# Kernel optimization log

Hardware: AMD Instinct MI355X
Metric: run time of the kernel (lower is better)

The kernel has to match this reference:

```python
import jax, jax.numpy as jnp
import numpy as np
import math

NUM_HEADS = 8
C_RATIO = 0.5

def _dwconv(x, w, b, pad):
    # x: [B,C,H,W], w: [C,1,kh,kw] depthwise
    y = jax.lax.conv_general_dilated(x, w, (1, 1), [(pad, pad), (pad, pad)],
                                     dimension_numbers=('NCHW', 'OIHW', 'NCHW'),
                                     feature_group_count=x.shape[1])
    return y + b[None, :, None, None]

def setup_inputs():
    key = jax.random.key(0)
    ks = jax.random.split(key, 16)
    B, H, W, C = 2, 128, 128, 384
    cr = int(C * C_RATIO)  # 192
    cg = C // 3            # 128
    s = 0.02
    return {
        'x': jax.random.normal(ks[0], (B, H * W, C), jnp.float32),
        'red_w1': jax.random.normal(ks[1], (cg, 1, 1, 1), jnp.float32) * s,
        'red_b1': jnp.zeros((cg,), jnp.float32),
        'red_w3': jax.random.normal(ks[2], (cg, 1, 3, 3), jnp.float32) * s,
        'red_b3': jnp.zeros((cg,), jnp.float32),
        'red_w5': jax.random.normal(ks[3], (cg, 1, 5, 5), jnp.float32) * s,
        'red_b5': jnp.zeros((cg,), jnp.float32),
        'fus_w': jax.random.normal(ks[4], (cr, C, 4, 4), jnp.float32) * s,
        'fus_b': jnp.zeros((cr,), jnp.float32),
        'q_w': jax.random.normal(ks[5], (C, cr), jnp.float32) * s,
        'k_w': jax.random.normal(ks[6], (cr, cr), jnp.float32) * s,
        'v_w': jax.random.normal(ks[7], (cr, C), jnp.float32) * s,
        'cpe_w': jax.random.normal(ks[8], (C, 1, 3, 3), jnp.float32) * s,
        'cpe_b': jnp.zeros((C,), jnp.float32),
        'proj_w': jax.random.normal(ks[9], (C, C), jnp.float32) * s,
        'proj_b': jnp.zeros((C,), jnp.float32),
        'H': 128,
        'W': 128,
    }

def reference(x, red_w1, red_b1, red_w3, red_b3, red_w5, red_b5,
              fus_w, fus_b, q_w, k_w, v_w, cpe_w, cpe_b, proj_w, proj_b, H, W):
    B, N, C = x.shape
    cr = q_w.shape[1]
    hd = C // NUM_HEADS
    dk = cr // NUM_HEADS
    scale = (hd * C_RATIO) ** -0.5
    _time = max(int(math.log(H // 16, 4)), int(math.log(W // 16, 4)))
    _scale = 4 ** _time  # == 4 for our shapes

    _x = x.transpose(0, 2, 1).reshape(B, C, H, W)
    x1, x2, x3 = jnp.split(_x, 3, axis=1)
    y1 = _dwconv(x1, red_w1, red_b1, 0)                       # applied once
    y2 = _dwconv(_dwconv(x2, red_w3, red_b3, 1), red_w3, red_b3, 1)  # twice
    y3 = x3
    for _ in range(3):                                        # thrice
        y3 = _dwconv(y3, red_w5, red_b5, 2)
    fused = jnp.concatenate([y1, y2, y3], axis=1)             # [B,C,H,W]

    f = jax.lax.conv_general_dilated(fused, fus_w, (4, 4), [(0, 0), (0, 0)],
                                     dimension_numbers=('NCHW', 'OIHW', 'NCHW'))
    f = jax.nn.gelu(f + fus_b[None, :, None, None], approximate=False)
    _xr = f.reshape(B, cr, -1).transpose(0, 2, 1)             # [B, L, cr], L = (H/4)*(W/4)

    q = (x @ q_w).reshape(B, N, NUM_HEADS, dk).transpose(0, 2, 1, 3)    # [B,h,N,dk]
    k = (_xr @ k_w).reshape(B, -1, NUM_HEADS, dk).transpose(0, 2, 1, 3) # [B,h,L,dk]
    v = (_xr @ v_w).reshape(B, -1, NUM_HEADS, hd).transpose(0, 2, 1, 3) # [B,h,L,hd]

    attn = jax.nn.softmax(jnp.einsum('bhnd,bhld->bhnl', q, k) * scale, axis=-1)

    Hs, Ws = H // _scale, W // _scale
    v_sp = v.transpose(0, 2, 1, 3).reshape(B, -1, C).transpose(0, 2, 1).reshape(B, C, Hs, Ws)
    v = v + _dwconv(v_sp, cpe_w, cpe_b, 1).reshape(B, C, -1).reshape(
        B, NUM_HEADS, hd, -1).transpose(0, 1, 3, 2)

    out = jnp.einsum('bhnl,bhld->bhnd', attn, v).transpose(0, 2, 1, 3).reshape(B, N, C)
    return out @ proj_w + proj_b
```

## Files before the change

kernel.cpp:

```cpp
#include <hip/hip_runtime.h>
#include <math.h>

typedef short short8 __attribute__((ext_vector_type(8)));
typedef float f32x4 __attribute__((ext_vector_type(4)));

#define B_    2
#define HH    128
#define WW    128
#define NPIX  16384
#define C_    384
#define CR    192
#define CG    128
#define NH    8
#define DK    24
#define HD    48
#define LL    1024
#define KFUS  6144
#define SCALE_L2E 0.29448889f

__device__ __forceinline__ float bf2f(short h) {
    union { unsigned u; float f; } v; v.u = ((unsigned)(unsigned short)h) << 16; return v.f;
}
__device__ __forceinline__ short f2bf(float f) {
    union { float f; unsigned u; } v; v.f = f;
    unsigned r = v.u + 0x7fffu + ((v.u >> 16) & 1u);
    return (short)(unsigned short)(r >> 16);
}
__device__ __forceinline__ short f2bf_fast(float f) {
    union { float f; unsigned u; } v; v.f = f;
    return (short)(unsigned short)((v.u + 0x8000u) >> 16);
}
__device__ __forceinline__ float exp2b(float x) {
#if __has_builtin(__builtin_amdgcn_exp2f)
    return __builtin_amdgcn_exp2f(x);
#else
    return exp2f(x);
#endif
}
__device__ __forceinline__ unsigned cvt_pk_bf16(float lo, float hi) {
    unsigned r;
    asm("v_cvt_pk_bf16_f32 %0, %1, %2" : "=v"(r) : "v"(lo), "v"(hi));
    return r;
}

template<int PATCH, int KS, int STRIDE>
__global__ __launch_bounds__(256) void dwconv_k(
    const float* __restrict__ in, int in_off,
    float* __restrict__ outf, short* __restrict__ outp, int out_coff,
    const float* __restrict__ w, const float* __restrict__ bias)
{
    constexpr int pad = KS / 2;
    constexpr int NV = 4 + KS - 1;
    int idx = blockIdx.x * 256 + threadIdx.x;
    int c    = idx & (CG - 1);
    int pix4 = (idx >> 7) & 4095;
    int b    = idx >> 19;
    int y = pix4 >> 5, x0 = (pix4 & 31) << 2;
    float wl[KS * KS];
    #pragma unroll
    for (int i = 0; i < KS * KS; i++) wl[i] = w[c * KS * KS + i];
    float bv = bias[c];
    float acc[4] = {bv, bv, bv, bv};
    #pragma unroll
    for (int ky = 0; ky < KS; ky++) {
        int yy = y + ky - pad;
        if ((unsigned)yy >= HH) continue;
        const float* rowp = &in[(size_t)(b * NPIX + yy * WW) * STRIDE + in_off + c];
        float v[NV];
        #pragma unroll
        for (int j = 0; j < NV; j++) {
            int xx = x0 + j - pad;
            v[j] = ((unsigned)xx < WW) ? rowp[(size_t)xx * STRIDE] : 0.f;
        }
        #pragma unroll
        for (int kx = 0; kx < KS; kx++)
            #pragma unroll
            for (int o = 0; o < 4; o++)
                acc[o] += v[o + kx] * wl[ky * KS + kx];
    }
    if (!PATCH) {
        float* op = &outf[(size_t)(b * NPIX + y * WW + x0) * CG + c];
        #pragma unroll
        for (int o = 0; o < 4; o++) op[(size_t)o * CG] = acc[o];
    } else {
        int m = b * LL + (y >> 2) * 32 + (x0 >> 2);
        short* op = &outp[(size_t)m * KFUS + ((y & 3) * 4) * C_ + out_coff + c];
        #pragma unroll
        for (int o = 0; o < 4; o++) op[(size_t)o * C_] = f2bf(acc[o]);
    }
}

__global__ __launch_bounds__(256) void prep_k(
    const float* __restrict__ fus_w, const float* __restrict__ k_w,
    const float* __restrict__ v_w, const float* __restrict__ q_w,
    const float* __restrict__ proj_w,
    short* __restrict__ Wt, short* __restrict__ Bkv,
    short* __restrict__ qw_b, short* __restrict__ pw_b)
{
    int idx = blockIdx.x * 256 + threadIdx.x;
    const int NW = KFUS * CR;
    if (idx < NW) {
        int k = idx / CR, oc = idx - k * CR;
        int p = k / C_,  ic = k - p * C_;
        Wt[idx] = f2bf(fus_w[(oc * C_ + ic) * 16 + p]);
        return;
    }
    idx -= NW;
    if (idx < CR * 576) {
        int k = idx / 576, n = idx - k * 576;
        Bkv[idx] = f2bf((n < CR) ? k_w[k * CR + n] : v_w[k * C_ + (n - CR)]);
        return;
    }
    idx -= CR * 576;
    if (idx < C_ * CR) { qw_b[idx] = f2bf(q_w[idx]); return; }
    idx -= C_ * CR;
    if (idx < C_ * C_) pw_b[idx] = f2bf(proj_w[idx]);
}

template<int AF, int CF>
__global__ __launch_bounds__(256) void gemm_k(
    const void* __restrict__ Av, const short* __restrict__ Bm, void* __restrict__ Cv,
    const float* __restrict__ bias, int M, int N, int K)
{
    __shared__ short a_lds[64 * 40];
    __shared__ short bT_lds[64 * 40];
    int tid = threadIdx.x;
    int lane = tid & 63, wave = tid >> 6, quad = lane >> 4, l16 = lane & 15;
    int bm = blockIdx.x * 64, bn = blockIdx.y * 64;
    int wm = (wave >> 1) * 32, wn = (wave & 1) * 32;
    f32x4 z4 = {0.f, 0.f, 0.f, 0.f};
    f32x4 acc00 = z4, acc01 = z4, acc10 = z4, acc11 = z4;
    int arow = tid >> 2, aseg = tid & 3;
    int bk = tid >> 3, bnseg = tid & 7;

    for (int k0 = 0; k0 < K; k0 += 32) {
        __syncthreads();
        if (AF) {
            const float* Af = (const float*)Av;
            const float4* p = (const float4*)&Af[(size_t)(bm + arow) * K + k0 + aseg * 8];
            float4 f0 = p[0], f1 = p[1];
            short8 av;
            av[0] = f2bf_fast(f0.x); av[1] = f2bf_fast(f0.y);
            av[2] = f2bf_fast(f0.z); av[3] = f2bf_fast(f0.w);
            av[4] = f2bf_fast(f1.x); av[5] = f2bf_fast(f1.y);
            av[6] = f2bf_fast(f1.z); av[7] = f2bf_fast(f1.w);
            *(short8*)&a_lds[arow * 40 + aseg * 8] = av;
        } else {
            const short* Ab = (const short*)Av;
            *(short8*)&a_lds[arow * 40 + aseg * 8] =
                *(const short8*)&Ab[(size_t)(bm + arow) * K + k0 + aseg * 8];
        }
        short8 bv = *(const short8*)&Bm[(size_t)(k0 + bk) * N + bn + bnseg * 8];
        #pragma unroll
        for (int i = 0; i < 8; i++) bT_lds[(bnseg * 8 + i) * 40 + bk] = bv[i];
        __syncthreads();
        short8 a0 = *(short8*)&a_lds[(wm + l16) * 40 + quad * 8];
        short8 a1 = *(short8*)&a_lds[(wm + 16 + l16) * 40 + quad * 8];
        short8 b0 = *(short8*)&bT_lds[(wn + l16) * 40 + quad * 8];
        short8 b1 = *(short8*)&bT_lds[(wn + 16 + l16) * 40 + quad * 8];
        acc00 = __builtin_amdgcn_mfma_f32_16x16x32_bf16(a0, b0, acc00, 0, 0, 0);
        acc01 = __builtin_amdgcn_mfma_f32_16x16x32_bf16(a0, b1, acc01, 0, 0, 0);
        acc10 = __builtin_amdgcn_mfma_f32_16x16x32_bf16(a1, b0, acc10, 0, 0, 0);
        acc11 = __builtin_amdgcn_mfma_f32_16x16x32_bf16(a1, b1, acc11, 0, 0, 0);
    }
    f32x4 accs[2][2] = {{acc00, acc01}, {acc10, acc11}};
    #pragma unroll
    for (int mt = 0; mt < 2; mt++)
      #pragma unroll
      for (int nt = 0; nt < 2; nt++) {
        int col = bn + wn + nt * 16 + l16;
        float bvv = bias ? bias[col] : 0.f;
        #pragma unroll
        for (int r = 0; r < 4; r++) {
            int row = bm + wm + mt * 16 + quad * 4 + r;
            float v = accs[mt][nt][r] + bvv;
            if (CF) ((float*)Cv)[(size_t)row * N + col] = v;
            else    ((short*)Cv)[(size_t)row * N + col] = f2bf(v);
        }
      }
}

__global__ __launch_bounds__(256) void gemm_part_k(
    const short* __restrict__ A, const short* __restrict__ Bm,
    float* __restrict__ Cpart, int M, int N, int K, int kchunk)
{
    __shared__ short a_lds[64 * 40];
    __shared__ short bT_lds[64 * 40];
    int tid = threadIdx.x;
    int lane = tid & 63, wave = tid >> 6, quad = lane >> 4, l16 = lane & 15;
    int bm = blockIdx.x * 64, bn = blockIdx.y * 64;
    int kbeg = blockIdx.z * kchunk, kend = kbeg + kchunk;
    int wm = (wave >> 1) * 32, wn = (wave & 1) * 32;
    f32x4 z4 = {0.f, 0.f, 0.f, 0.f};
    f32x4 acc00 = z4, acc01 = z4, acc10 = z4, acc11 = z4;
    int arow = tid >> 2, aseg = tid & 3;
    int bk = tid >> 3, bnseg = tid & 7;

    for (int k0 = kbeg; k0 < kend; k0 += 32) {
        __syncthreads();
        *(short8*)&a_lds[arow * 40 + aseg * 8] =
            *(const short8*)&A[(size_t)(bm + arow) * K + k0 + aseg * 8];
        short8 bv = *(const short8*)&Bm[(size_t)(k0 + bk) * N + bn + bnseg * 8];
        #pragma unroll
        for (int i = 0; i < 8; i++) bT_lds[(bnseg * 8 + i) * 40 + bk] = bv[i];
        __syncthreads();
        short8 a0 = *(short8*)&a_lds[(wm + l16) * 40 + quad * 8];
        short8 a1 = *(short8*)&a_lds[(wm + 16 + l16) * 40 + quad * 8];
        short8 b0 = *(short8*)&bT_lds[(wn + l16) * 40 + quad * 8];
        short8 b1 = *(short8*)&bT_lds[(wn + 16 + l16) * 40 + quad * 8];
        acc00 = __builtin_amdgcn_mfma_f32_16x16x32_bf16(a0, b0, acc00, 0, 0, 0);
        acc01 = __builtin_amdgcn_mfma_f32_16x16x32_bf16(a0, b1, acc01, 0, 0, 0);
        acc10 = __builtin_amdgcn_mfma_f32_16x16x32_bf16(a1, b0, acc10, 0, 0, 0);
        acc11 = __builtin_amdgcn_mfma_f32_16x16x32_bf16(a1, b1, acc11, 0, 0, 0);
    }
    float* Cs = Cpart + (size_t)blockIdx.z * M * N;
    f32x4 accs[2][2] = {{acc00, acc01}, {acc10, acc11}};
    #pragma unroll
    for (int mt = 0; mt < 2; mt++)
      #pragma unroll
      for (int nt = 0; nt < 2; nt++) {
        int col = bn + wn + nt * 16 + l16;
        #pragma unroll
        for (int r = 0; r < 4; r++) {
            int row = bm + wm + mt * 16 + quad * 4 + r;
            Cs[(size_t)row * N + col] = accs[mt][nt][r];
        }
      }
}

__global__ __launch_bounds__(256) void fusred_k(
    const float* __restrict__ part, const float* __restrict__ bias,
    short* __restrict__ xr)
{
    const int MN = 2048 * CR;
    int idx = blockIdx.x * 256 + threadIdx.x;
    float v = part[idx] + part[idx + MN] + part[idx + 2 * MN] + part[idx + 3 * MN]
            + bias[idx % CR];
    v = 0.5f * v * (1.f + erff(v * 0.70710678118f));
    xr[idx] = f2bf(v);
}

__global__ __launch_bounds__(256) void cpe_k(
    const short* __restrict__ kv, const float* __restrict__ cw,
    const float* __restrict__ cb, short* __restrict__ v2)
{
    int idx = blockIdx.x * 256 + threadIdx.x;
    int c8 = idx % 48;
    int t  = idx / 48;
    int l  = t & (LL - 1);
    int b  = t >> 10;
    int c0 = c8 * 8;
    int y = l >> 5, x = l & 31;
    const short* vp = kv + CR;
    float acc[8];
    {
        short8 v0 = *(const short8*)&vp[(size_t)(b * LL + l) * 576 + c0];
        #pragma unroll
        for (int i = 0; i < 8; i++) acc[i] = bf2f(v0[i]) + cb[c0 + i];
    }
    #pragma unroll
    for (int ky = 0; ky < 3; ky++) {
        int yy = y + ky - 1; if ((unsigned)yy >= 32) continue;
        #pragma unroll
        for (int kx = 0; kx < 3; kx++) {
            int xx = x + kx - 1; if ((unsigned)xx >= 32) continue;
            short8 nv = *(const short8*)&vp[(size_t)(b * LL + yy * 32 + xx) * 576 + c0];
            #pragma unroll
            for (int i = 0; i < 8; i++)
                acc[i] += bf2f(nv[i]) * cw[(c0 + i) * 9 + ky * 3 + kx];
        }
    }
    short8 ov;
    #pragma unroll
    for (int i = 0; i < 8; i++) ov[i] = f2bf(acc[i]);
    *(short8*)&v2[(size_t)(b * LL + l) * C_ + c0] = ov;
}

__global__ __launch_bounds__(256) void transp_k(
    const short* __restrict__ v2b, const short* __restrict__ kvb,
    short* __restrict__ v2t, short* __restrict__ kpack)
{
    int tid = threadIdx.x;
    if (blockIdx.x < 256) {
        __shared__ short t_lds[64 * 49];
        int bh = blockIdx.x >> 4, b = bh >> 3, h = bh & 7;
        int l0 = (blockIdx.x & 15) << 6;
        for (int i = tid; i < 64 * 48; i += 256) {
            int dl = i / 48, f = i - dl * 48;
            t_lds[dl * 49 + f] = v2b[(size_t)(b * LL + l0 + dl) * C_ + h * HD + f];
        }
        __syncthreads();
        for (int i = tid; i < 64 * 48; i += 256) {
            int f = i >> 6, dl = i & 63;
            int l = l0 + dl;
            v2t[(size_t)bh * 49152 + (size_t)((l >> 5) * 3 + (f >> 4)) * 512
                + (f & 15) * 32 + (l & 31)] = t_lds[dl * 49 + f];
        }
    } else {
        int gid = (blockIdx.x - 256) * 256 + tid;
        int j = gid & 31, t = gid >> 5;
        int l = t & (LL - 1), bh = t >> 10;
        int b = bh >> 3, h = bh & 7;
        int jj = l & 31, a = jj >> 3, c = jj & 7;
        int s = (c < 4) ? (a * 4 + c) : (16 + a * 4 + (c - 4));
        int lp = (l & ~31) | s;
        kpack[(size_t)bh * 32768 + lp * 32 + j] =
            (j < 24) ? kvb[(size_t)(b * LL + l) * 576 + h * DK + j] : (short)0;
    }
}

__global__ __launch_bounds__(256, 4) void attn_k(
    const short* __restrict__ qbuf, const short* __restrict__ kpack,
    const short* __restrict__ v2t, short* __restrict__ obuf)
{
    int tid = threadIdx.x;
    int lane = tid & 63, wave = tid >> 6, quad = lane >> 4, l16 = lane & 15;
    int bh = blockIdx.y, b = bh >> 3, h = bh & 7;
    int q0 = blockIdx.x * 128 + wave * 32;

    short8 qf[2];
    #pragma unroll
    for (int qt = 0; qt < 2; qt++) {
        short8 z = {0, 0, 0, 0, 0, 0, 0, 0};
        qf[qt] = z;
        if (quad < 3) {
            short8 raw = *(const short8*)&qbuf[(size_t)(b * NPIX + q0 + qt * 16 + l16) * CR + h * DK + quad * 8];
            #pragma unroll
            for (int i = 0; i < 8; i++) qf[qt][i] = f2bf(bf2f(raw[i]) * SCALE_L2E);
        }
    }

    f32x4 z4 = {0.f, 0.f, 0.f, 0.f};
    f32x4 oacc[2][3] = {{z4, z4, z4}, {z4, z4, z4}};
    float rs[2] = {0.f, 0.f};

    const short* kp = kpack + (((size_t)bh) << 15) + l16 * 32 + quad * 8;
    const short* vt = v2t + (size_t)bh * 49152 + l16 * 32 + quad * 8;

    short8 kf1 = *(const short8*)&kp[0];
    short8 kf2 = *(const short8*)&kp[512];

    for (int kt = 0; kt < 32; kt++) {
        short8 av0 = *(const short8*)&vt[(kt * 3) << 9];
        short8 av1 = *(const short8*)&vt[(kt * 3 + 1) << 9];
        short8 av2 = *(const short8*)&vt[(kt * 3 + 2) << 9];
        int ktn = (kt + 1) & 31;
        short8 nk1 = *(const short8*)&kp[ktn << 10];
        short8 nk2 = *(const short8*)&kp[(ktn << 10) + 512];
        #pragma unroll
        for (int qt = 0; qt < 2; qt++) {
            f32x4 s1 = __builtin_amdgcn_mfma_f32_16x16x32_bf16(kf1, qf[qt], z4, 0, 0, 0);
            f32x4 s2 = __builtin_amdgcn_mfma_f32_16x16x32_bf16(kf2, qf[qt], z4, 0, 0, 0);
            float e0 = exp2b(s1[0]), e1 = exp2b(s1[1]);
            float e2 = exp2b(s1[2]), e3 = exp2b(s1[3]);
            float g0 = exp2b(s2[0]), g1 = exp2b(s2[1]);
            float g2 = exp2b(s2[2]), g3 = exp2b(s2[3]);
            rs[qt] += ((e0 + e1) + (e2 + e3)) + ((g0 + g1) + (g2 + g3));
            union { unsigned u[4]; short8 s; } pb;
            pb.u[0] = cvt_pk_bf16(e0, e1);
            pb.u[1] = cvt_pk_bf16(e2, e3);
            pb.u[2] = cvt_pk_bf16(g0, g1);
            pb.u[3] = cvt_pk_bf16(g2, g3);
            oacc[qt][0] = __builtin_amdgcn_mfma_f32_16x16x32_bf16(av0, pb.s, oacc[qt][0], 0, 0, 0);
            oacc[qt][1] = __builtin_amdgcn_mfma_f32_16x16x32_bf16(av1, pb.s, oacc[qt][1], 0, 0, 0);
            oacc[qt][2] = __builtin_amdgcn_mfma_f32_16x16x32_bf16(av2, pb.s, oacc[qt][2], 0, 0, 0);
        }
        kf1 = nk1; kf2 = nk2;
    }

    #pragma unroll
    for (int qt = 0; qt < 2; qt++) {
        float s = rs[qt];
        s += __shfl_xor(s, 16);
        s += __shfl_xor(s, 32);
        float inv = 1.0f / s;
        short* orow = &obuf[(size_t)(b * NPIX + q0 + qt * 16 + l16) * C_ + h * HD + quad * 4];
        #pragma unroll
        for (int nt = 0; nt < 3; nt++) {
            uint2 ov;
            ov.x = cvt_pk_bf16(oacc[qt][nt][0] * inv, oacc[qt][nt][1] * inv);
            ov.y = cvt_pk_bf16(oacc[qt][nt][2] * inv, oacc[qt][nt][3] * inv);
            *(uint2*)&orow[nt * 16] = ov;
        }
    }
}

extern "C" void kernel_launch(void* const* d_in, const int* in_sizes, int n_in,
                              void* d_out, int out_size, void* d_ws, size_t ws_size,
                              hipStream_t stream)
{
    const float* x      = (const float*)d_in[0];
    const float* red_w1 = (const float*)d_in[1];
    const float* red_b1 = (const float*)d_in[2];
    const float* red_w3 = (const float*)d_in[3];
    const float* red_b3 = (const float*)d_in[4];
    const float* red_w5 = (const float*)d_in[5];
    const float* red_b5 = (const float*)d_in[6];
    const float* fus_w  = (const float*)d_in[7];
    const float* fus_b  = (const float*)d_in[8];
    const float* q_w    = (const float*)d_in[9];
    const float* k_w    = (const float*)d_in[10];
    const float* v_w    = (const float*)d_in[11];
    const float* cpe_w  = (const float*)d_in[12];
    const float* cpe_b  = (const float*)d_in[13];
    const float* proj_w = (const float*)d_in[14];
    const float* proj_b = (const float*)d_in[15];
    float* out = (float*)d_out;

    char* ws = (char*)d_ws;
    short* A_fus = (short*)(ws +         0);
    short* obuf  = A_fus;
    float* tmpA  = (float*)(ws +  25165824);
    short* qbuf  = (short*)(ws +  25165824);
    float* tmpB  = (float*)(ws +  41943040);
    float* part  = (float*)(ws +  41943040);
    short* v2t   = (short*)(ws +  48234496);
    short* kpack = (short*)(ws +  49807360);
    short* Wt    = (short*)(ws +  58720256);
    short* Bkv   = (short*)(ws +  61079552);
    short* qw_b  = (short*)(ws +  61300736);
    short* pw_b  = (short*)(ws +  61448192);
    short* xr    = (short*)(ws +  61743104);
    short* kvb   = (short*)(ws +  62529536);
    short* v2b   = (short*)(ws +  64888832);
    (void)in_sizes; (void)n_in; (void)out_size; (void)ws_size;

    dim3 blk(256);
    dwconv_k<1,1,C_><<<dim3(4096), blk, 0, stream>>>(x,    0,   nullptr, A_fus, 0,   red_w1, red_b1);
    dwconv_k<0,3,C_><<<dim3(4096), blk, 0, stream>>>(x,    128, tmpA,  nullptr, 0,   red_w3, red_b3);
    dwconv_k<1,3,CG><<<dim3(4096), blk, 0, stream>>>(tmpA, 0,   nullptr, A_fus, 128, red_w3, red_b3);
    dwconv_k<0,5,C_><<<dim3(4096), blk, 0, stream>>>(x,    256, tmpB,  nullptr, 0,   red_w5, red_b5);
    dwconv_k<0,5,CG><<<dim3(4096), blk, 0, stream>>>(tmpB, 0,   tmpA,  nullptr, 0,   red_w5, red_b5);
    dwconv_k<1,5,CG><<<dim3(4096), blk, 0, stream>>>(tmpA, 0,   nullptr, A_fus, 256, red_w5, red_b5);
    prep_k<<<dim3(5904), blk, 0, stream>>>(fus_w, k_w, v_w, q_w, proj_w, Wt, Bkv, qw_b, pw_b);
    gemm_part_k<<<dim3(32, 3, 4), blk, 0, stream>>>(A_fus, Wt, part, 2048, CR, KFUS, KFUS / 4);
    fusred_k<<<dim3(1536), blk, 0, stream>>>(part, fus_b, xr);
    gemm_k<0,0><<<dim3(32, 9), blk, 0, stream>>>(xr, Bkv, kvb, (const float*)nullptr, 2048, 576, CR);
    cpe_k<<<dim3(384), blk, 0, stream>>>(kvb, cpe_w, cpe_b, v2b);
    transp_k<<<dim3(2304), blk, 0, stream>>>(v2b, kvb, v2t, kpack);
    gemm_k<1,0><<<dim3(512, 3), blk, 0, stream>>>(x, qw_b, qbuf, (const float*)nullptr, 32768, CR, C_);
    attn_k<<<dim3(128, 16), blk, 0, stream>>>(qbuf, kpack, v2t, obuf);
    gemm_k<0,1><<<dim3(512, 6), blk, 0, stream>>>(obuf, pw_b, out, proj_b, 32768, C_, C_);
}
```

Measured before the change: 419.2 us.

## Merge independent first-stage convs with weight prep and enlarge attention query tiles

The three depthwise convs that read x directly and the weight-conversion prep are merged into one launch, dispatched by block index, so fewer kernels run and they overlap. The GEMM grids are swapped so consecutive blocks share the same A rows across N tiles, which should improve L2 reuse. Each attention wave now handles 64 queries instead of 32, and V fragments are prefetched one tile ahead like K, so each K/V load is reused more. The larger attention tile raises register pressure and halves the number of attention blocks.

```diff
diff --git a/kernel.cpp b/kernel.cpp
--- a/kernel.cpp
+++ b/kernel.cpp
@@ -44,14 +44,14 @@
 }
 
 template<int PATCH, int KS, int STRIDE>
-__global__ __launch_bounds__(256) void dwconv_k(
+__device__ __forceinline__ void dwconv_body(
+    int idx,
     const float* __restrict__ in, int in_off,
     float* __restrict__ outf, short* __restrict__ outp, int out_coff,
     const float* __restrict__ w, const float* __restrict__ bias)
 {
     constexpr int pad = KS / 2;
     constexpr int NV = 4 + KS - 1;
-    int idx = blockIdx.x * 256 + threadIdx.x;
     int c    = idx & (CG - 1);
     int pix4 = (idx >> 7) & 4095;
     int b    = idx >> 19;
@@ -90,14 +90,24 @@
     }
 }
 
-__global__ __launch_bounds__(256) void prep_k(
+template<int PATCH, int KS, int STRIDE>
+__global__ __launch_bounds__(256) void dwconv_k(
+    const float* __restrict__ in, int in_off,
+    float* __restrict__ outf, short* __restrict__ outp, int out_coff,
+    const float* __restrict__ w, const float* __restrict__ bias)
+{
+    dwconv_body<PATCH, KS, STRIDE>(blockIdx.x * 256 + threadIdx.x,
+                                   in, in_off, outf, outp, out_coff, w, bias);
+}
+
+__device__ __forceinline__ void prep_body(
+    int idx,
     const float* __restrict__ fus_w, const float* __restrict__ k_w,
     const float* __restrict__ v_w, const float* __restrict__ q_w,
     const float* __restrict__ proj_w,
     short* __restrict__ Wt, short* __restrict__ Bkv,
     short* __restrict__ qw_b, short* __restrict__ pw_b)
 {
-    int idx = blockIdx.x * 256 + threadIdx.x;
     const int NW = KFUS * CR;
     if (idx < NW) {
         int k = idx / CR, oc = idx - k * CR;
@@ -117,7 +127,31 @@
     if (idx < C_ * C_) pw_b[idx] = f2bf(proj_w[idx]);
 }
 
-template<int AF, int CF>
+__global__ __launch_bounds__(256) void stage1_k(
+    const float* __restrict__ x, short* __restrict__ A_fus,
+    float* __restrict__ tmpA, float* __restrict__ tmpB,
+    const float* __restrict__ red_w1, const float* __restrict__ red_b1,
+    const float* __restrict__ red_w3, const float* __restrict__ red_b3,
+    const float* __restrict__ red_w5, const float* __restrict__ red_b5,
+    const float* __restrict__ fus_w, const float* __restrict__ k_w,
+    const float* __restrict__ v_w, const float* __restrict__ q_w,
+    const float* __restrict__ proj_w,
+    short* __restrict__ Wt, short* __restrict__ Bkv,
+    short* __restrict__ qw_b, short* __restrict__ pw_b)
+{
+    int bx = blockIdx.x;
+    if (bx < 4096) {
+        dwconv_body<1,1,C_>(bx * 256 + threadIdx.x, x, 0, nullptr, A_fus, 0, red_w1, red_b1);
+    } else if (bx < 8192) {
+        dwconv_body<0,3,C_>((bx - 4096) * 256 + threadIdx.x, x, 128, tmpA, nullptr, 0, red_w3, red_b3);
+    } else if (bx < 12288) {
+        dwconv_body<0,5,C_>((bx - 8192) * 256 + threadIdx.x, x, 256, tmpB, nullptr, 0, red_w5, red_b5);
+    } else {
+        prep_body((bx - 12288) * 256 + threadIdx.x, fus_w, k_w, v_w, q_w, proj_w, Wt, Bkv, qw_b, pw_b);
+    }
+}
+
+template<int AF, int CF, int SWAP = 0>
 __global__ __launch_bounds__(256) void gemm_k(
     const void* __restrict__ Av, const short* __restrict__ Bm, void* __restrict__ Cv,
     const float* __restrict__ bias, int M, int N, int K)
@@ -126,7 +160,8 @@
     __shared__ short bT_lds[64 * 40];
     int tid = threadIdx.x;
     int lane = tid & 63, wave = tid >> 6, quad = lane >> 4, l16 = lane & 15;
-    int bm = blockIdx.x * 64, bn = blockIdx.y * 64;
+    int bm = (SWAP ? blockIdx.y : blockIdx.x) * 64;
+    int bn = (SWAP ? blockIdx.x : blockIdx.y) * 64;
     int wm = (wave >> 1) * 32, wn = (wave & 1) * 32;
     f32x4 z4 = {0.f, 0.f, 0.f, 0.f};
     f32x4 acc00 = z4, acc01 = z4, acc10 = z4, acc11 = z4;
@@ -188,7 +223,7 @@
     __shared__ short bT_lds[64 * 40];
     int tid = threadIdx.x;
     int lane = tid & 63, wave = tid >> 6, quad = lane >> 4, l16 = lane & 15;
-    int bm = blockIdx.x * 64, bn = blockIdx.y * 64;
+    int bm = blockIdx.y * 64, bn = blockIdx.x * 64;
     int kbeg = blockIdx.z * kchunk, kend = kbeg + kchunk;
     int wm = (wave >> 1) * 32, wn = (wave & 1) * 32;
     f32x4 z4 = {0.f, 0.f, 0.f, 0.f};
@@ -316,11 +351,11 @@
     int tid = threadIdx.x;
     int lane = tid & 63, wave = tid >> 6, quad = lane >> 4, l16 = lane & 15;
     int bh = blockIdx.y, b = bh >> 3, h = bh & 7;
-    int q0 = blockIdx.x * 128 + wave * 32;
-
-    short8 qf[2];
-    #pragma unroll
-    for (int qt = 0; qt < 2; qt++) {
+    int q0 = blockIdx.x * 256 + wave * 64;
+
+    short8 qf[4];
+    #pragma unroll
+    for (int qt = 0; qt < 4; qt++) {
         short8 z = {0, 0, 0, 0, 0, 0, 0, 0};
         qf[qt] = z;
         if (quad < 3) {
@@ -331,24 +366,27 @@
     }
 
     f32x4 z4 = {0.f, 0.f, 0.f, 0.f};
-    f32x4 oacc[2][3] = {{z4, z4, z4}, {z4, z4, z4}};
-    float rs[2] = {0.f, 0.f};
+    f32x4 oacc[4][3] = {{z4, z4, z4}, {z4, z4, z4}, {z4, z4, z4}, {z4, z4, z4}};
+    float rs[4] = {0.f, 0.f, 0.f, 0.f};
 
     const short* kp = kpack + (((size_t)bh) << 15) + l16 * 32 + quad * 8;
     const short* vt = v2t + (size_t)bh * 49152 + l16 * 32 + quad * 8;
 
     short8 kf1 = *(const short8*)&kp[0];
     short8 kf2 = *(const short8*)&kp[512];
+    short8 av0 = *(const short8*)&vt[0];
+    short8 av1 = *(const short8*)&vt[512];
+    short8 av2 = *(const short8*)&vt[1024];
 
     for (int kt = 0; kt < 32; kt++) {
-        short8 av0 = *(const short8*)&vt[(kt * 3) << 9];
-        short8 av1 = *(const short8*)&vt[(kt * 3 + 1) << 9];
-        short8 av2 = *(const short8*)&vt[(kt * 3 + 2) << 9];
         int ktn = (kt + 1) & 31;
         short8 nk1 = *(const short8*)&kp[ktn << 10];
         short8 nk2 = *(const short8*)&kp[(ktn << 10) + 512];
-        #pragma unroll
-        for (int qt = 0; qt < 2; qt++) {
+        short8 nv0 = *(const short8*)&vt[(ktn * 3) << 9];
+        short8 nv1 = *(const short8*)&vt[((ktn * 3 + 1)) << 9];
+        short8 nv2 = *(const short8*)&vt[((ktn * 3 + 2)) << 9];
+        #pragma unroll
+        for (int qt = 0; qt < 4; qt++) {
             f32x4 s1 = __builtin_amdgcn_mfma_f32_16x16x32_bf16(kf1, qf[qt], z4, 0, 0, 0);
             f32x4 s2 = __builtin_amdgcn_mfma_f32_16x16x32_bf16(kf2, qf[qt], z4, 0, 0, 0);
             float e0 = exp2b(s1[0]), e1 = exp2b(s1[1]);
@@ -365,11 +403,11 @@
             oacc[qt][1] = __builtin_amdgcn_mfma_f32_16x16x32_bf16(av1, pb.s, oacc[qt][1], 0, 0, 0);
             oacc[qt][2] = __builtin_amdgcn_mfma_f32_16x16x32_bf16(av2, pb.s, oacc[qt][2], 0, 0, 0);
         }
-        kf1 = nk1; kf2 = nk2;
-    }
-
-    #pragma unroll
-    for (int qt = 0; qt < 2; qt++) {
+        kf1 = nk1; kf2 = nk2; av0 = nv0; av1 = nv1; av2 = nv2;
+    }
+
+    #pragma unroll
+    for (int qt = 0; qt < 4; qt++) {
         float s = rs[qt];
         s += __shfl_xor(s, 16);
         s += __shfl_xor(s, 32);
@@ -426,19 +464,18 @@
     (void)in_sizes; (void)n_in; (void)out_size; (void)ws_size;
 
     dim3 blk(256);
-    dwconv_k<1,1,C_><<<dim3(4096), blk, 0, stream>>>(x,    0,   nullptr, A_fus, 0,   red_w1, red_b1);
-    dwconv_k<0,3,C_><<<dim3(4096), blk, 0, stream>>>(x,    128, tmpA,  nullptr, 0,   red_w3, red_b3);
-    dwconv_k<1,3,CG><<<dim3(4096), blk, 0, stream>>>(tmpA, 0,   nullptr, A_fus, 128, red_w3, red_b3);
-    dwconv_k<0,5,C_><<<dim3(4096), blk, 0, stream>>>(x,    256, tmpB,  nullptr, 0,   red_w5, red_b5);
-    dwconv_k<0,5,CG><<<dim3(4096), blk, 0, stream>>>(tmpB, 0,   tmpA,  nullptr, 0,   red_w5, red_b5);
-    dwconv_k<1,5,CG><<<dim3(4096), blk, 0, stream>>>(tmpA, 0,   nullptr, A_fus, 256, red_w5, red_b5);
-    prep_k<<<dim3(5904), blk, 0, stream>>>(fus_w, k_w, v_w, q_w, proj_w, Wt, Bkv, qw_b, pw_b);
-    gemm_part_k<<<dim3(32, 3, 4), blk, 0, stream>>>(A_fus, Wt, part, 2048, CR, KFUS, KFUS / 4);
+    stage1_k<<<dim3(18192), blk, 0, stream>>>(
+        x, A_fus, tmpA, tmpB, red_w1, red_b1, red_w3, red_b3, red_w5, red_b5,
+        fus_w, k_w, v_w, q_w, proj_w, Wt, Bkv, qw_b, pw_b);
+    dwconv_k<1,3,CG><<<dim3(4096), blk, 0, stream>>>(tmpA, 0, nullptr, A_fus, 128, red_w3, red_b3);
+    dwconv_k<0,5,CG><<<dim3(4096), blk, 0, stream>>>(tmpB, 0, tmpA,  nullptr, 0,   red_w5, red_b5);
+    dwconv_k<1,5,CG><<<dim3(4096), blk, 0, stream>>>(tmpA, 0, nullptr, A_fus, 256, red_w5, red_b5);
+    gemm_part_k<<<dim3(3, 32, 4), blk, 0, stream>>>(A_fus, Wt, part, 2048, CR, KFUS, KFUS / 4);
     fusred_k<<<dim3(1536), blk, 0, stream>>>(part, fus_b, xr);
     gemm_k<0,0><<<dim3(32, 9), blk, 0, stream>>>(xr, Bkv, kvb, (const float*)nullptr, 2048, 576, CR);
     cpe_k<<<dim3(384), blk, 0, stream>>>(kvb, cpe_w, cpe_b, v2b);
     transp_k<<<dim3(2304), blk, 0, stream>>>(v2b, kvb, v2t, kpack);
-    gemm_k<1,0><<<dim3(512, 3), blk, 0, stream>>>(x, qw_b, qbuf, (const float*)nullptr, 32768, CR, C_);
-    attn_k<<<dim3(128, 16), blk, 0, stream>>>(qbuf, kpack, v2t, obuf);
-    gemm_k<0,1><<<dim3(512, 6), blk, 0, stream>>>(obuf, pw_b, out, proj_b, 32768, C_, C_);
-}
+    gemm_k<1,0,1><<<dim3(3, 512), blk, 0, stream>>>(x, qw_b, qbuf, (const float*)nullptr, 32768, CR, C_);
+    attn_k<<<dim3(64, 16), blk, 0, stream>>>(qbuf, kpack, v2t, obuf);
+    gemm_k<0,1,1><<<dim3(6, 512), blk, 0, stream>>>(obuf, pw_b, out, proj_b, 32768, C_, C_);
+}
```

Result: faster. 399.8 us (-4.6%).
